# Kernel tuning notes

Hardware: AMD Instinct MI355X
Metric: run time of the kernel (lower is better)

## Reference

```python
import jax, jax.numpy as jnp
import numpy as np

B, IN_LEN, NN, IN_DIM = 32, 28, 2048, 1
E, ND = 256, 256          # embed_dim, node_dim
H = E + ND                # hidden_dim = 512
N_LAYERS = 3
OUT_LEN = 28


def setup_inputs() -> dict:
    key = jax.random.key(0)
    ks = jax.random.split(key, 16)
    x_node = jax.random.normal(ks[0], (B, IN_LEN, NN, IN_DIM), jnp.float32)
    # x_state channels: [0]=cumulative cases, [1]=infected I, [2]=population N
    col0 = jax.random.uniform(ks[1], (B, IN_LEN, NN, 1), jnp.float32) * 100.0
    colI = jax.random.uniform(ks[2], (B, IN_LEN, NN, 1), jnp.float32) * 100.0 + 1.0
    colN = 1e4 * (1.0 + 0.1 * jax.random.uniform(ks[3], (B, IN_LEN, NN, 1), jnp.float32))
    x_state = jnp.concatenate([col0, colI, colN], axis=-1)
    node_emb = jax.random.normal(ks[4], (NN, ND), jnp.float32) * 0.05
    W_ts = jax.random.normal(ks[5], (E, IN_DIM * IN_LEN), jnp.float32) * 0.05
    b_ts = jnp.zeros((E,), jnp.float32)
    enc_W1 = jax.random.normal(ks[6], (N_LAYERS, H, H), jnp.float32) * 0.02
    enc_b1 = jnp.zeros((N_LAYERS, H), jnp.float32)
    enc_W2 = jax.random.normal(ks[7], (N_LAYERS, H, H), jnp.float32) * 0.02
    enc_b2 = jnp.zeros((N_LAYERS, H), jnp.float32)
    Wb = jax.random.normal(ks[8], (1, H), jnp.float32) * 0.05
    bb = jnp.zeros((1,), jnp.float32)
    Wg = jax.random.normal(ks[9], (1, H), jnp.float32) * 0.05
    bg = jnp.zeros((1,), jnp.float32)
    return dict(x_node=x_node, x_state=x_state, node_emb=node_emb,
                W_ts=W_ts, b_ts=b_ts, enc_W1=enc_W1, enc_b1=enc_b1,
                enc_W2=enc_W2, enc_b2=enc_b2, Wb=Wb, bb=bb, Wg=Wg, bg=bg)


def _forward(x_node, x_state, node_emb, W_ts, b_ts,
             enc_W1, enc_b1, enc_W2, enc_b2, Wb, bb, Wg, bg):
    Bn, Lh, Nn, _ = x_node.shape
    # [B,L,N,D] -> [B,N,L*D] (channel = in_dim*in_len for 1x1 conv == linear)
    flat = jnp.transpose(x_node[..., :IN_DIM], (0, 2, 1, 3)).reshape(Bn, Nn, Lh * IN_DIM)
    ts = flat @ W_ts.T + b_ts                                  # [B,N,E]
    h = jnp.concatenate(
        [ts, jnp.broadcast_to(node_emb[None], (Bn,) + node_emb.shape)], axis=-1)  # [B,N,H]
    for l in range(enc_W1.shape[0]):                            # residual MLP encoder
        z = jnp.maximum(h @ enc_W1[l].T + enc_b1[l], 0.0)
        h = h + z @ enc_W2[l].T + enc_b2[l]
    b = jax.nn.sigmoid(h @ Wb.T + bb)                           # [B,N,1] infection rate
    g = jax.nn.sigmoid(h @ Wg.T + bg)                           # [B,N,1] recovery rate

    Npop = x_state[:, -1, :, 2:3]                               # [B,N,1]
    I_hist = x_state[..., 1:2] / g[:, None]                     # [B,L,N,1]
    Iin_hist = jnp.maximum(
        I_hist[:, 1:] - I_hist[:, :-1] + x_state[:, :-1, :, 1:2], 0.0)  # [B,L-1,N,1]
    t1 = jnp.arange(Lh - 1, 0, -1, dtype=jnp.float32)
    w1 = jnp.exp(-g[:, None] * t1[None, :, None, None])         # [B,L-1,N,1]
    I_Tm1 = jnp.sum(w1 * Iin_hist, axis=1)                      # [B,N,1]
    R_Tm1 = Npop - x_state[:, -2, :, 0:1]
    S_Tm1 = Npop - I_Tm1 - R_Tm1
    Iin0 = b * S_Tm1 * I_Tm1 / Npop
    Rin0 = g * I_hist[:, -1, :, 0:1]
    Iin_hist = jnp.concatenate([Iin_hist, Iin0[:, None]], axis=1)  # [B,L,N,1]
    S = S_Tm1 - Iin0
    t2 = jnp.arange(Lh, 0, -1, dtype=jnp.float32)
    w2 = jnp.exp(-g[:, None] * t2[None, :, None, None])
    I = jnp.sum(w2 * Iin_hist, axis=1)                          # [B,N,1]
    R = R_Tm1 + Rin0

    # The torch loop recomputes sum_i exp(-g*(L-i))*Iin_i each step; exact identity:
    # I_new = exp(-g) * (I_old + Iin_new). O(T) scan instead of O(T^2).
    decay = jnp.exp(-g)

    def step(carry, _):
        S, I, R = carry
        Iin = b * S * I / Npop
        S = S - Iin
        Rin = g * I            # uses pre-update I_T, matching torch order
        I = decay * (I + Iin)
        R = R + Rin
        return (S, I, R), Rin

    _, rins = jax.lax.scan(step, (S, I, R), None, length=OUT_LEN)  # [T,B,N,1]
    return jnp.transpose(rins, (1, 0, 2, 3))                       # [B,out_len,N,1]


def reference(x_node, x_state, node_emb, W_ts, b_ts, enc_W1, enc_b1,
              enc_W2, enc_b2, Wb, bb, Wg, bg):
    return _forward(x_node, x_state, node_emb, W_ts, b_ts,
                    enc_W1, enc_b1, enc_W2, enc_b2, Wb, bb, Wg, bg)
```

## Files before the change

kernel.cpp:

```cpp
#include <hip/hip_runtime.h>
#include <hip/hip_bf16.h>
#include <math.h>

#define BATCH 32
#define IN_LEN 28
#define NN 2048
#define E 256
#define H 512
#define N_LAYERS 3
#define OUT_LEN 28
#define M_ROWS (BATCH * NN)

typedef unsigned short u16;
typedef unsigned int   u32;
typedef __attribute__((ext_vector_type(8))) short short8;
typedef __attribute__((ext_vector_type(4))) float f32x4;

__device__ __forceinline__ u16 f2h(float x) {
    union { _Float16 h; u16 u; } v; v.h = (_Float16)x; return v.u;
}
__device__ __forceinline__ float h2f(u16 u) {
    union { _Float16 h; u16 u; } v; v.u = u; return (float)v.h;
}

__device__ __forceinline__ void gload_lds16(const void* g, void* l) {
    __builtin_amdgcn_global_load_lds(
        (const __attribute__((address_space(1))) void*)g,
        (__attribute__((address_space(3))) void*)l, 16, 0, 0);
}

__global__ __launch_bounds__(256)
void k_split2(const float* __restrict__ w1, const float* __restrict__ w2,
              u16* __restrict__ hi, u16* __restrict__ lo, int nW)
{
    int i = blockIdx.x * 256 + threadIdx.x;
    float v = (i < nW) ? w1[i] : w2[i - nW];
    u16 h = f2h(v);
    hi[i] = h;
    lo[i] = f2h(v - h2f(h));
}

__global__ __launch_bounds__(256)
void k_ts(const float* __restrict__ x_node, const float* __restrict__ node_emb,
          const float* __restrict__ W_ts, const float* __restrict__ b_ts,
          u16* __restrict__ hhi, u16* __restrict__ hlo)
{
    __shared__ float xs[IN_LEN][64];
    const int tid = threadIdx.x;
    const int b   = blockIdx.y;
    const int n0  = blockIdx.x * 64;

    for (int idx = tid; idx < IN_LEN * 64; idx += 256) {
        int l = idx >> 6, i = idx & 63;
        xs[l][i] = x_node[((size_t)b * IN_LEN + l) * NN + n0 + i];
    }
    __syncthreads();

    float w[IN_LEN];
    #pragma unroll
    for (int j = 0; j < IN_LEN; j++) w[j] = W_ts[tid * IN_LEN + j];
    const float bias = b_ts[tid];

    for (int i = 0; i < 64; i++) {
        float acc = bias;
        #pragma unroll
        for (int j = 0; j < IN_LEN; j++) acc += xs[j][i] * w[j];
        size_t row = (size_t)b * NN + n0 + i;
        u16 thi = f2h(acc);
        hhi[row * H + tid] = thi;
        hlo[row * H + tid] = f2h(acc - h2f(thi));
        float ev = node_emb[(size_t)(n0 + i) * 256 + tid];
        u16 ehi = f2h(ev);
        hhi[row * H + E + tid] = ehi;
        hlo[row * H + E + tid] = f2h(ev - h2f(ehi));
    }
}

__global__ __launch_bounds__(256)
void k_gemm1(const u16* __restrict__ Ahi, const u16* __restrict__ Alo,
             const u16* __restrict__ Whi, const u16* __restrict__ Wlo,
             const float* __restrict__ bias, u16* __restrict__ Z)
{
    __shared__ __align__(16) u16 smem[32768];

    const int tid = threadIdx.x;
    const int ln  = tid & 63;
    const int wv  = tid >> 6;

    const int id   = blockIdx.x;
    const int c    = (id >> 3) & 3;
    const int r    = (id & 7) | ((id >> 5) << 3);
    const int row0 = r * 128;
    const int col0 = c * 128;

    const int rbase = (wv & 1) * 64;
    const int cbase = (wv >> 1) * 64;

    const int lr = ln >> 2;
    const int lc = ln & 3;

    const u16* sgsrc; int sofs; int tb;
    if      (wv == 0) { sgsrc = Ahi; sofs = 0;     tb = row0; }
    else if (wv == 1) { sgsrc = Alo; sofs = 8192;  tb = row0; }
    else if (wv == 2) { sgsrc = Whi; sofs = 16384; tb = col0; }
    else              { sgsrc = Wlo; sofs = 24576; tb = col0; }

    auto stage = [&](int p, int kt) {
        u16* dstbuf = smem + sofs + p * 4096;
        #pragma unroll
        for (int i = 0; i < 8; i++) {
            int row = i * 16 + lr;
            int sc  = lc ^ ((row >> 1) & 3);
            gload_lds16(sgsrc + (size_t)(tb + row) * H + kt + sc * 8,
                        dstbuf + i * 512);
        }
    };

    f32x4 acc[4][4];
    #pragma unroll
    for (int m = 0; m < 4; m++)
        #pragma unroll
        for (int n = 0; n < 4; n++) acc[m][n] = (f32x4)(0.f);

    stage(0, 0);

    const int wl = ln & 15;

    for (int t = 0; t < 16; t++) {
        const int p = t & 1;
        __syncthreads();
        if (t + 1 < 16) stage(1 - p, (t + 1) * 32);

        const u16* bAh = smem + 0     + p * 4096;
        const u16* bAl = smem + 8192  + p * 4096;
        const u16* bWh = smem + 16384 + p * 4096;
        const u16* bWl = smem + 24576 + p * 4096;

        short8 ahi[4], alo[4], whi[4], wlo[4];
        #pragma unroll
        for (int m = 0; m < 4; m++) {
            int rr = rbase + m * 16 + wl;
            int cc = ((ln >> 4) ^ ((rr >> 1) & 3)) * 8;
            ahi[m] = *(const short8*)&bAh[rr * 32 + cc];
            alo[m] = *(const short8*)&bAl[rr * 32 + cc];
        }
        #pragma unroll
        for (int n = 0; n < 4; n++) {
            int wr = cbase + n * 16 + wl;
            int cc = ((ln >> 4) ^ ((wr >> 1) & 3)) * 8;
            whi[n] = *(const short8*)&bWh[wr * 32 + cc];
            wlo[n] = *(const short8*)&bWl[wr * 32 + cc];
        }
        #pragma unroll
        for (int m = 0; m < 4; m++)
            #pragma unroll
            for (int n = 0; n < 4; n++) {
                acc[m][n] = __builtin_amdgcn_mfma_f32_16x16x32_f16(ahi[m], whi[n], acc[m][n], 0, 0, 0);
                acc[m][n] = __builtin_amdgcn_mfma_f32_16x16x32_f16(ahi[m], wlo[n], acc[m][n], 0, 0, 0);
                acc[m][n] = __builtin_amdgcn_mfma_f32_16x16x32_f16(alo[m], whi[n], acc[m][n], 0, 0, 0);
            }
    }

    __syncthreads();
    u16* zb = smem + wv * 4096;
    float bv[4];
    #pragma unroll
    for (int n = 0; n < 4; n++) bv[n] = bias[col0 + cbase + n * 16 + wl];
    #pragma unroll
    for (int m = 0; m < 4; m++)
        #pragma unroll
        for (int n = 0; n < 4; n++)
            #pragma unroll
            for (int rg = 0; rg < 4; rg++) {
                int row_l = m * 16 + (ln >> 4) * 4 + rg;
                zb[row_l * 64 + n * 16 + wl] =
                    f2h(fmaxf(acc[m][n][rg] + bv[n], 0.f));
            }
    const int cr = ln >> 3;
    const int cc = (ln & 7) * 8;
    #pragma unroll
    for (int p2 = 0; p2 < 8; p2++) {
        int row_l = cr + p2 * 8;
        uint4 v = *(const uint4*)&zb[row_l * 64 + cc];
        *(uint4*)&Z[(size_t)(row0 + rbase + row_l) * H + col0 + cbase + cc] = v;
    }
}

template <int HEAD>
__global__ __launch_bounds__(256)
void k_gemm2(const u16* __restrict__ Z,
             const u16* __restrict__ Whi, const u16* __restrict__ Wlo,
             const float* __restrict__ bias,
             u16* HHi, u16* HLo,
             const float* __restrict__ Wb, const float* __restrict__ Wg,
             float* __restrict__ bSum, float* __restrict__ gSum)
{
    __shared__ __align__(16) u16 smem[24576];

    const int tid = threadIdx.x;
    const int ln  = tid & 63;
    const int wv  = tid >> 6;

    const int id   = blockIdx.x;
    const int c    = (id >> 3) & 3;
    const int r    = (id & 7) | ((id >> 5) << 3);
    const int row0 = r * 128;
    const int col0 = c * 128;

    const int rbase = (wv & 1) * 64;
    const int cbase = (wv >> 1) * 64;

    const int lr = ln >> 2;
    const int lc = ln & 3;

    const u16* sgsrc; int sofs; int tb; int iofs; int niss;
    if      (wv == 0) { sgsrc = Z;   sofs = 0;     tb = row0;      iofs = 0;    niss = 4; }
    else if (wv == 3) { sgsrc = Z;   sofs = 0;     tb = row0 + 64; iofs = 2048; niss = 4; }
    else if (wv == 1) { sgsrc = Whi; sofs = 8192;  tb = col0;      iofs = 0;    niss = 8; }
    else              { sgsrc = Wlo; sofs = 16384; tb = col0;      iofs = 0;    niss = 8; }

    auto stage = [&](int p, int kt) {
        u16* dstbuf = smem + sofs + p * 4096 + iofs;
        #pragma unroll
        for (int i = 0; i < 8; i++) {
            if (i >= niss) break;
            int row = i * 16 + lr;
            int sc  = lc ^ ((row >> 1) & 3);
            gload_lds16(sgsrc + (size_t)(tb + row) * H + kt + sc * 8,
                        dstbuf + i * 512);
        }
    };

    f32x4 acc[4][4];
    #pragma unroll
    for (int m = 0; m < 4; m++)
        #pragma unroll
        for (int n = 0; n < 4; n++) acc[m][n] = (f32x4)(0.f);

    stage(0, 0);

    const int wl = ln & 15;

    for (int t = 0; t < 16; t++) {
        const int p = t & 1;
        __syncthreads();
        if (t + 1 < 16) stage(1 - p, (t + 1) * 32);

        const u16* bZ  = smem + 0     + p * 4096;
        const u16* bWh = smem + 8192  + p * 4096;
        const u16* bWl = smem + 16384 + p * 4096;

        short8 az[4], whi[4], wlo[4];
        #pragma unroll
        for (int m = 0; m < 4; m++) {
            int rr = rbase + m * 16 + wl;
            int cc = ((ln >> 4) ^ ((rr >> 1) & 3)) * 8;
            az[m] = *(const short8*)&bZ[rr * 32 + cc];
        }
        #pragma unroll
        for (int n = 0; n < 4; n++) {
            int wr = cbase + n * 16 + wl;
            int cc = ((ln >> 4) ^ ((wr >> 1) & 3)) * 8;
            whi[n] = *(const short8*)&bWh[wr * 32 + cc];
            wlo[n] = *(const short8*)&bWl[wr * 32 + cc];
        }
        #pragma unroll
        for (int m = 0; m < 4; m++)
            #pragma unroll
            for (int n = 0; n < 4; n++) {
                acc[m][n] = __builtin_amdgcn_mfma_f32_16x16x32_f16(az[m], whi[n], acc[m][n], 0, 0, 0);
                acc[m][n] = __builtin_amdgcn_mfma_f32_16x16x32_f16(az[m], wlo[n], acc[m][n], 0, 0, 0);
            }
    }

    __syncthreads();
    float* fb = (float*)smem + wv * 2048;

    const int cr  = ln >> 3;
    const int ccl = (ln & 7) * 4;
    float pb[8], pg[8];
    if (HEAD) {
        #pragma unroll
        for (int p2 = 0; p2 < 8; p2++) { pb[p2] = 0.f; pg[p2] = 0.f; }
    }

    #pragma unroll
    for (int nh = 0; nh < 2; nh++) {
        #pragma unroll
        for (int m = 0; m < 4; m++)
            #pragma unroll
            for (int j = 0; j < 2; j++)
                #pragma unroll
                for (int rg = 0; rg < 4; rg++) {
                    int row_l = m * 16 + (ln >> 4) * 4 + rg;
                    fb[row_l * 32 + j * 16 + wl] = acc[m][nh * 2 + j][rg];
                }
        const int gc0 = col0 + cbase + nh * 32 + ccl;
        float4 bv = *(const float4*)&bias[gc0];
        float4 hb, hg;
        if (HEAD) {
            hb = *(const float4*)&Wb[gc0];
            hg = *(const float4*)&Wg[gc0];
        }
        #pragma unroll
        for (int p2 = 0; p2 < 8; p2++) {
            int row_l = cr + p2 * 8;
            size_t gidx = (size_t)(row0 + rbase + row_l) * H + gc0;
            uint2 uh = *(const uint2*)(HHi + gidx);
            uint2 ul = *(const uint2*)(HLo + gidx);
            float4 a = *(const float4*)&fb[row_l * 32 + ccl];
            float v0 = a.x + bv.x + h2f((u16)(uh.x & 0xFFFF)) + h2f((u16)(ul.x & 0xFFFF));
            float v1 = a.y + bv.y + h2f((u16)(uh.x >> 16))    + h2f((u16)(ul.x >> 16));
            float v2 = a.z + bv.z + h2f((u16)(uh.y & 0xFFFF)) + h2f((u16)(ul.y & 0xFFFF));
            float v3 = a.w + bv.w + h2f((u16)(uh.y >> 16))    + h2f((u16)(ul.y >> 16));
            if (HEAD) {
                pb[p2] += v0 * hb.x + v1 * hb.y + v2 * hb.z + v3 * hb.w;
                pg[p2] += v0 * hg.x + v1 * hg.y + v2 * hg.z + v3 * hg.w;
            }
            u16 h0 = f2h(v0), h1 = f2h(v1), h2 = f2h(v2), h3 = f2h(v3);
            uint2 oh, ol;
            oh.x = (u32)h0 | ((u32)h1 << 16);
            oh.y = (u32)h2 | ((u32)h3 << 16);
            ol.x = (u32)f2h(v0 - h2f(h0)) | ((u32)f2h(v1 - h2f(h1)) << 16);
            ol.y = (u32)f2h(v2 - h2f(h2)) | ((u32)f2h(v3 - h2f(h3)) << 16);
            *(uint2*)(HHi + gidx) = oh;
            *(uint2*)(HLo + gidx) = ol;
        }
    }

    if (HEAD) {
        #pragma unroll
        for (int p2 = 0; p2 < 8; p2++) {
            float sb = pb[p2], sg = pg[p2];
            #pragma unroll
            for (int off = 1; off < 8; off <<= 1) {
                sb += __shfl_xor(sb, off);
                sg += __shfl_xor(sg, off);
            }
            if ((ln & 7) == 0) {
                int grow = row0 + rbase + cr + p2 * 8;
                atomicAdd(&bSum[grow], sb);
                atomicAdd(&gSum[grow], sg);
            }
        }
    }
}

__global__ __launch_bounds__(256)
void k_sir(const float* __restrict__ x_state,
           const float* __restrict__ bSum, const float* __restrict__ gSum,
           const float* __restrict__ bb, const float* __restrict__ bg,
           float* __restrict__ out)
{
    const int row = blockIdx.x * 256 + threadIdx.x;
    const int bb_ = row / NN;
    const int n   = row % NN;

    const float g = 1.f / (1.f + expf(-(gSum[row] + bg[0])));
    const float b = 1.f / (1.f + expf(-(bSum[row] + bb[0])));
    const float d = expf(-g);

    const float* xs = x_state + ((size_t)bb_ * IN_LEN) * (NN * 3) + (size_t)n * 3;

    float x1_prev = xs[1];
    float Ih_prev = x1_prev / g;
    float acc = 0.f;
    #pragma unroll 4
    for (int t = 1; t <= IN_LEN - 1; ++t) {
        float x1 = xs[(size_t)t * (NN * 3) + 1];
        float Ih = x1 / g;
        float Iin = fmaxf(Ih - Ih_prev + x1_prev, 0.f);
        acc = acc * d + Iin;
        Ih_prev = Ih;
        x1_prev = x1;
    }
    float ITm1 = acc * d;
    float Npop = xs[(size_t)(IN_LEN - 1) * (NN * 3) + 2];
    float RTm1 = Npop - xs[(size_t)(IN_LEN - 2) * (NN * 3) + 0];
    float STm1 = Npop - ITm1 - RTm1;
    float Iin0 = b * STm1 * ITm1 / Npop;
    float S = STm1 - Iin0;
    float I = d * (ITm1 + Iin0);

    float* op = out + ((size_t)bb_ * OUT_LEN) * NN + n;
    #pragma unroll 4
    for (int k = 0; k < OUT_LEN; k++) {
        float Iin = b * S * I / Npop;
        S = S - Iin;
        float Rin = g * I;
        I = d * (I + Iin);
        op[(size_t)k * NN] = Rin;
    }
}

extern "C" void kernel_launch(void* const* d_in, const int* in_sizes, int n_in,
                              void* d_out, int out_size, void* d_ws, size_t ws_size,
                              hipStream_t stream)
{
    const float* x_node   = (const float*)d_in[0];
    const float* x_state  = (const float*)d_in[1];
    const float* node_emb = (const float*)d_in[2];
    const float* W_ts     = (const float*)d_in[3];
    const float* b_ts     = (const float*)d_in[4];
    const float* enc_W1   = (const float*)d_in[5];
    const float* enc_b1   = (const float*)d_in[6];
    const float* enc_W2   = (const float*)d_in[7];
    const float* enc_b2   = (const float*)d_in[8];
    const float* Wb       = (const float*)d_in[9];
    const float* bb       = (const float*)d_in[10];
    const float* Wg       = (const float*)d_in[11];
    const float* bg       = (const float*)d_in[12];
    float* out = (float*)d_out;

    u16* hhi   = (u16*)d_ws;
    u16* hlo   = hhi + (size_t)M_ROWS * H;
    u16* wHi   = hlo + (size_t)M_ROWS * H;
    u16* wLo   = wHi + (size_t)6 * H * H;
    float* bSum = (float*)(wLo + (size_t)6 * H * H);
    float* gSum = bSum + M_ROWS;
    u16* z     = (u16*)(gSum + M_ROWS);

    size_t used  = (size_t)((char*)z - (char*)d_ws);
    size_t avail = (ws_size > used) ? ws_size - used : 0;
    long long chunkLL = (long long)(avail / (H * sizeof(u16))) & ~1023LL;
    int chunk = (chunkLL > M_ROWS) ? M_ROWS : (int)chunkLL;
    if (chunk < 1024) chunk = 1024;

    hipMemsetAsync(bSum, 0, 2 * (size_t)M_ROWS * sizeof(float), stream);

    const int nW = N_LAYERS * H * H;
    k_split2<<<2 * nW / 256, 256, 0, stream>>>(enc_W1, enc_W2, wHi, wLo, nW);

    k_ts<<<dim3(NN / 64, BATCH), 256, 0, stream>>>(x_node, node_emb, W_ts, b_ts, hhi, hlo);

    for (int l = 0; l < N_LAYERS; l++) {
        const u16* W1hi = wHi + (size_t)l * H * H;
        const u16* W1lo = wLo + (size_t)l * H * H;
        const u16* W2hi = wHi + (size_t)nW + (size_t)l * H * H;
        const u16* W2lo = wLo + (size_t)nW + (size_t)l * H * H;
        const float* b1 = enc_b1 + (size_t)l * H;
        const float* b2 = enc_b2 + (size_t)l * H;
        for (int r = 0; r < M_ROWS; r += chunk) {
            int rows = (M_ROWS - r < chunk) ? (M_ROWS - r) : chunk;
            u16* hrhi = hhi + (size_t)r * H;
            u16* hrlo = hlo + (size_t)r * H;
            int nblk = (rows / 128) * 4;
            k_gemm1<<<nblk, 256, 0, stream>>>(hrhi, hrlo, W1hi, W1lo, b1, z);
            if (l < N_LAYERS - 1)
                k_gemm2<0><<<nblk, 256, 0, stream>>>(z, W2hi, W2lo, b2, hrhi, hrlo,
                                                     Wb, Wg, bSum, gSum);
            else
                k_gemm2<1><<<nblk, 256, 0, stream>>>(z, W2hi, W2lo, b2, hrhi, hrlo,
                                                     Wb, Wg, bSum, gSum);
        }
    }

    k_sir<<<M_ROWS / 256, 256, 0, stream>>>(x_state, bSum, gSum, bb, bg, out);
}
```

Before: 787.5 us.

## Process rows in L2-sized chunks across all layers and vectorize embedding kernel

The row-chunk loop becomes the outer loop and the layer loop the inner one, with chunks capped at 32768 rows. Each chunk's hidden state and Z buffer can then stay cached while all three encoder layers run over it, instead of streaming the full activation through memory once per layer. Offsets into bSum/gSum are added so chunked output lands in the right rows; without them the old code looks like it wrote to the wrong place when more than one chunk ran. The ts/embedding kernel also splits its threads into two halves, one for the time-series projection and one for the embedding copy, each writing packed pairs of fp16 values. The cost is more kernel launches when the full problem used to fit in one chunk.

```diff
diff --git a/kernel.cpp b/kernel.cpp
--- a/kernel.cpp
+++ b/kernel.cpp
@@ -49,30 +49,50 @@
     const int tid = threadIdx.x;
     const int b   = blockIdx.y;
     const int n0  = blockIdx.x * 64;
+    const int c   = tid & 127;
+    const int sec = tid >> 7;
 
     for (int idx = tid; idx < IN_LEN * 64; idx += 256) {
         int l = idx >> 6, i = idx & 63;
         xs[l][i] = x_node[((size_t)b * IN_LEN + l) * NN + n0 + i];
     }
+
+    float w0[IN_LEN], w1[IN_LEN];
+    float bias0 = 0.f, bias1 = 0.f;
+    if (sec == 0) {
+        #pragma unroll
+        for (int j = 0; j < IN_LEN; j++) {
+            w0[j] = W_ts[(2 * c) * IN_LEN + j];
+            w1[j] = W_ts[(2 * c + 1) * IN_LEN + j];
+        }
+        bias0 = b_ts[2 * c];
+        bias1 = b_ts[2 * c + 1];
+    }
     __syncthreads();
 
-    float w[IN_LEN];
-    #pragma unroll
-    for (int j = 0; j < IN_LEN; j++) w[j] = W_ts[tid * IN_LEN + j];
-    const float bias = b_ts[tid];
-
     for (int i = 0; i < 64; i++) {
-        float acc = bias;
-        #pragma unroll
-        for (int j = 0; j < IN_LEN; j++) acc += xs[j][i] * w[j];
         size_t row = (size_t)b * NN + n0 + i;
-        u16 thi = f2h(acc);
-        hhi[row * H + tid] = thi;
-        hlo[row * H + tid] = f2h(acc - h2f(thi));
-        float ev = node_emb[(size_t)(n0 + i) * 256 + tid];
-        u16 ehi = f2h(ev);
-        hhi[row * H + E + tid] = ehi;
-        hlo[row * H + E + tid] = f2h(ev - h2f(ehi));
+        u32* oh = (u32*)(hhi + row * H);
+        u32* ol = (u32*)(hlo + row * H);
+        float v0, v1;
+        int oc;
+        if (sec == 0) {
+            v0 = bias0; v1 = bias1;
+            #pragma unroll
+            for (int j = 0; j < IN_LEN; j++) {
+                float x = xs[j][i];
+                v0 += x * w0[j];
+                v1 += x * w1[j];
+            }
+            oc = c;
+        } else {
+            const float2 ev = *(const float2*)&node_emb[(size_t)(n0 + i) * 256 + 2 * c];
+            v0 = ev.x; v1 = ev.y;
+            oc = 128 + c;
+        }
+        u16 h0 = f2h(v0), h1 = f2h(v1);
+        oh[oc] = (u32)h0 | ((u32)h1 << 16);
+        ol[oc] = (u32)f2h(v0 - h2f(h0)) | ((u32)f2h(v1 - h2f(h1)) << 16);
     }
 }
 
@@ -425,6 +445,7 @@
     long long chunkLL = (long long)(avail / (H * sizeof(u16))) & ~1023LL;
     int chunk = (chunkLL > M_ROWS) ? M_ROWS : (int)chunkLL;
     if (chunk < 1024) chunk = 1024;
+    if (chunk > 32768) chunk = 32768;
 
     hipMemsetAsync(bSum, 0, 2 * (size_t)M_ROWS * sizeof(float), stream);
 
@@ -433,25 +454,25 @@
 
     k_ts<<<dim3(NN / 64, BATCH), 256, 0, stream>>>(x_node, node_emb, W_ts, b_ts, hhi, hlo);
 
-    for (int l = 0; l < N_LAYERS; l++) {
-        const u16* W1hi = wHi + (size_t)l * H * H;
-        const u16* W1lo = wLo + (size_t)l * H * H;
-        const u16* W2hi = wHi + (size_t)nW + (size_t)l * H * H;
-        const u16* W2lo = wLo + (size_t)nW + (size_t)l * H * H;
-        const float* b1 = enc_b1 + (size_t)l * H;
-        const float* b2 = enc_b2 + (size_t)l * H;
-        for (int r = 0; r < M_ROWS; r += chunk) {
-            int rows = (M_ROWS - r < chunk) ? (M_ROWS - r) : chunk;
-            u16* hrhi = hhi + (size_t)r * H;
-            u16* hrlo = hlo + (size_t)r * H;
-            int nblk = (rows / 128) * 4;
+    for (int r = 0; r < M_ROWS; r += chunk) {
+        int rows = (M_ROWS - r < chunk) ? (M_ROWS - r) : chunk;
+        u16* hrhi = hhi + (size_t)r * H;
+        u16* hrlo = hlo + (size_t)r * H;
+        int nblk = (rows / 128) * 4;
+        for (int l = 0; l < N_LAYERS; l++) {
+            const u16* W1hi = wHi + (size_t)l * H * H;
+            const u16* W1lo = wLo + (size_t)l * H * H;
+            const u16* W2hi = wHi + (size_t)nW + (size_t)l * H * H;
+            const u16* W2lo = wLo + (size_t)nW + (size_t)l * H * H;
+            const float* b1 = enc_b1 + (size_t)l * H;
+            const float* b2 = enc_b2 + (size_t)l * H;
             k_gemm1<<<nblk, 256, 0, stream>>>(hrhi, hrlo, W1hi, W1lo, b1, z);
             if (l < N_LAYERS - 1)
                 k_gemm2<0><<<nblk, 256, 0, stream>>>(z, W2hi, W2lo, b2, hrhi, hrlo,
-                                                     Wb, Wg, bSum, gSum);
+                                                     Wb, Wg, bSum + r, gSum + r);
             else
                 k_gemm2<1><<<nblk, 256, 0, stream>>>(z, W2hi, W2lo, b2, hrhi, hrlo,
-                                                     Wb, Wg, bSum, gSum);
+                                                     Wb, Wg, bSum + r, gSum + r);
         }
     }
 
```

After: 843.3 us. 1.07x slower.
